# Kernel optimization log

Hardware: AMD Instinct MI355X
Metric: run time of the kernel (lower is better)

The kernel has to match this reference:

```python
import jax, jax.numpy as jnp
import numpy as np


def _mlp(x, W1, b1, W2, b2, W3, b3):
    # flatten -> fc(784,512) -> relu -> fc(512,128) -> relu -> fc(128,C)
    h = x.reshape(x.shape[0], -1)
    h = jax.nn.relu(h @ W1.T + b1)
    h = jax.nn.relu(h @ W2.T + b2)
    return h @ W3.T + b3


def setup_inputs() -> dict:
    key = jax.random.key(0)
    ks = jax.random.split(key, 6)
    B, Bu, C, D = 65536, 4096, 10, 28 * 28
    return {
        "x": jax.random.uniform(ks[0], (B, 28, 28), jnp.float32),
        "y": jax.random.randint(ks[1], (B,), 0, C),
        "x_unlab": jax.random.uniform(ks[2], (Bu, 28, 28), jnp.float32),
        "W1": jax.random.normal(ks[3], (512, D), jnp.float32) * 0.03,
        "b1": jnp.zeros((512,), jnp.float32),
        "W2": jax.random.normal(ks[4], (128, 512), jnp.float32) * 0.05,
        "b2": jnp.zeros((128,), jnp.float32),
        "W3": jax.random.normal(ks[5], (C, 128), jnp.float32) * 0.08,
        "b3": jnp.zeros((C,), jnp.float32),
    }


def reference(x, y, x_unlab, W1, b1, W2, b2, W3, b3):
    n_classes = W3.shape[0]
    # ---- labeled branch: BCEWithLogitsLoss(mean) vs one-hot targets ----
    logits = _mlp(x, W1, b1, W2, b2, W3, b3)  # [B, C]
    t = jax.nn.one_hot(y, n_classes, dtype=logits.dtype)
    bce = jnp.mean(jnp.maximum(logits, 0.0) - logits * t
                   + jnp.log1p(jnp.exp(-jnp.abs(logits))))
    # ---- unlabeled branch: semantic loss ----
    # sem_loss(probs): s[c] = sum_i p_i[c] * prod_{j != i} (1 - p_j[c]);
    # return mean over classes of -log(s). Done in log domain with a single
    # O(Bu) leave-one-out sum instead of the original O(Bu^2) double loop.
    o_u = _mlp(x_unlab, W1, b1, W2, b2, W3, b3)       # [Bu, C]
    logp = jax.nn.log_sigmoid(o_u)                     # log p
    log1mp = jax.nn.log_sigmoid(-o_u)                  # log (1 - p)
    loo = jnp.sum(log1mp, axis=0, keepdims=True) - log1mp  # leave-one-out log-prod
    log_s = jax.scipy.special.logsumexp(logp + loo, axis=0)  # [C]
    sl = jnp.mean(-log_s)
    # compute_loss returns (bce, sl); stacked here as a length-2 vector
    return jnp.stack([bce, sl])
```

## Files before the change

kernel.cpp:

```cpp
#include <hip/hip_runtime.h>
#include <hip/hip_bf16.h>
#include <stdint.h>

typedef unsigned short ushort_t;
typedef __bf16 bf16x8 __attribute__((ext_vector_type(8)));
typedef float f32x4 __attribute__((ext_vector_type(4)));

__device__ __forceinline__ ushort_t f2bf(float f) {
    union { float f; unsigned u; } v; v.f = f;
    unsigned u = v.u;
    unsigned r = u + 0x7fffu + ((u >> 16) & 1u);
    return (ushort_t)(r >> 16);
}
__device__ __forceinline__ float bf2f(ushort_t h) {
    union { unsigned u; float f; } v; v.u = ((unsigned)h) << 16;
    return v.f;
}
__device__ __forceinline__ uint4 pack8(float4 a, float4 b) {
    uint4 r;
    r.x = ((unsigned)f2bf(a.y) << 16) | f2bf(a.x);
    r.y = ((unsigned)f2bf(a.w) << 16) | f2bf(a.z);
    r.z = ((unsigned)f2bf(b.y) << 16) | f2bf(b.x);
    r.w = ((unsigned)f2bf(b.w) << 16) | f2bf(b.z);
    return r;
}

#define GLDS16(gsrc, ldst)                                                    \
    __builtin_amdgcn_global_load_lds(                                         \
        (const __attribute__((address_space(1))) void*)(gsrc),                \
        (__attribute__((address_space(3))) void*)(ldst), 16, 0, 0)

__global__ __launch_bounds__(256) void prep_kernel(
    const float* __restrict__ W1, const float* __restrict__ W2,
    ushort_t* __restrict__ W1p, ushort_t* __restrict__ W2b,
    float* __restrict__ stats)
{
    int idx = blockIdx.x * 256 + threadIdx.x;
    if (idx < 512 * 800) {
        int n = idx / 800, k = idx - n * 800;
        W1p[idx] = (k < 784) ? f2bf(W1[n * 784 + k]) : (ushort_t)0;
    }
    if (idx < 128 * 512) W2b[idx] = f2bf(W2[idx]);
    if (idx == 0) stats[0] = 0.0f;
}

__global__ __launch_bounds__(256) void gemm1f_kernel(
    const float* __restrict__ x, const float* __restrict__ xu,
    const ushort_t* __restrict__ W1p, const float* __restrict__ b1,
    ushort_t* __restrict__ h1)
{
    __shared__ ushort_t As[2][128 * 32];
    __shared__ ushort_t Bs[2][128 * 32];

    const int b = blockIdx.x;
    const int xcd = b & 7, s = b >> 3;
    const int tile_n = s & 3;
    const int tile_m = xcd * 68 + (s >> 2);

    const int tid = threadIdx.x;
    const int w = tid >> 6, lane = tid & 63;
    const int wm = w >> 1, wn = w & 1;
    const int quad = lane >> 4, lc = lane & 15;
    const int row_in = lane >> 2;
    const int koff = (lane & 3) * 8;

    const int arow = tid >> 1;
    const int akoff = (tid & 1) * 16;
    const int grow = tile_m * 128 + arow;
    const float* asrc = (grow < 65536) ? (x + (size_t)grow * 784)
                                       : (xu + (size_t)(grow - 65536) * 784);

    const ushort_t* bsrc0 =
        W1p + (size_t)(tile_n * 128 + (w * 2 + 0) * 16 + row_in) * 800 + koff;
    const ushort_t* bsrc1 =
        W1p + (size_t)(tile_n * 128 + (w * 2 + 1) * 16 + row_in) * 800 + koff;

    f32x4 acc[4][4];
#pragma unroll
    for (int i = 0; i < 4; i++)
#pragma unroll
        for (int j = 0; j < 4; j++)
#pragma unroll
            for (int r = 0; r < 4; r++) acc[i][j][r] = 0.0f;

    float4 pa0, pa1, pa2, pa3;

    GLDS16(bsrc0, &Bs[0][(w * 2 + 0) * 512]);
    GLDS16(bsrc1, &Bs[0][(w * 2 + 1) * 512]);
    {
        const float4* q = (const float4*)(asrc + akoff);
        float4 a0 = q[0], a1 = q[1], a2 = q[2], a3 = q[3];
        *(uint4*)&As[0][arow * 32 + akoff]     = pack8(a0, a1);
        *(uint4*)&As[0][arow * 32 + akoff + 8] = pack8(a2, a3);
    }
    {
        const float4* q = (const float4*)(asrc + 32 + akoff);
        pa0 = q[0]; pa1 = q[1]; pa2 = q[2]; pa3 = q[3];
    }
    __syncthreads();

    for (int t = 0; t < 25; ++t) {
        const int cur = t & 1;
        if (t < 24) {
            ushort_t* Asn = &As[cur ^ 1][0];
            ushort_t* Bsn = &Bs[cur ^ 1][0];
            const int kb = (t + 1) * 32;
            GLDS16(bsrc0 + kb, &Bsn[(w * 2 + 0) * 512]);
            GLDS16(bsrc1 + kb, &Bsn[(w * 2 + 1) * 512]);
            uint4 lo, hi;
            if (kb + akoff <= 768) {
                lo = pack8(pa0, pa1);
                hi = pack8(pa2, pa3);
            } else {
                lo = make_uint4(0, 0, 0, 0);
                hi = make_uint4(0, 0, 0, 0);
            }
            *(uint4*)&Asn[arow * 32 + akoff]     = lo;
            *(uint4*)&Asn[arow * 32 + akoff + 8] = hi;
            const int kn = (t + 2) * 32 + akoff;
            if (t < 23 && kn <= 768) {
                const float4* q = (const float4*)(asrc + kn);
                pa0 = q[0]; pa1 = q[1]; pa2 = q[2]; pa3 = q[3];
            }
        }
        {
            bf16x8 af[4], bfr[4];
#pragma unroll
            for (int i = 0; i < 4; i++)
                af[i] = *(const bf16x8*)&As[cur][(wm * 64 + i * 16 + lc) * 32 + quad * 8];
#pragma unroll
            for (int j = 0; j < 4; j++)
                bfr[j] = *(const bf16x8*)&Bs[cur][(wn * 64 + j * 16 + lc) * 32 + quad * 8];
#pragma unroll
            for (int i = 0; i < 4; i++)
#pragma unroll
                for (int j = 0; j < 4; j++)
                    acc[i][j] = __builtin_amdgcn_mfma_f32_16x16x32_bf16(
                        af[i], bfr[j], acc[i][j], 0, 0, 0);
        }
        if (t < 24) __syncthreads();
    }

    float bias[4];
#pragma unroll
    for (int j = 0; j < 4; j++)
        bias[j] = b1[tile_n * 128 + wn * 64 + j * 16 + lc];
#pragma unroll
    for (int i = 0; i < 4; i++) {
        int gr0 = tile_m * 128 + wm * 64 + i * 16 + quad * 4;
#pragma unroll
        for (int j = 0; j < 4; j++) {
            int gc = tile_n * 128 + wn * 64 + j * 16 + lc;
#pragma unroll
            for (int r = 0; r < 4; r++) {
                float v = acc[i][j][r] + bias[j];
                v = fmaxf(v, 0.0f);
                h1[(size_t)(gr0 + r) * 512 + gc] = f2bf(v);
            }
        }
    }
}

__global__ __launch_bounds__(256) void gemm23_kernel(
    const ushort_t* __restrict__ h1, const ushort_t* __restrict__ W2b,
    const float* __restrict__ b2, const int* __restrict__ y,
    const float* __restrict__ W3, const float* __restrict__ b3,
    float* __restrict__ stats, float* __restrict__ logits_u)
{
    __shared__ ushort_t As[2][64 * 32];
    __shared__ ushort_t Bs[2][128 * 32];
    __shared__ float W3s[1280];
    __shared__ float b3s[10];
    __shared__ float red[4];

    const int tid = threadIdx.x;
    const int w = tid >> 6, lane = tid & 63;
    const int wm = w >> 1, wn = w & 1;
    const int quad = lane >> 4, lc = lane & 15;
    const int row_in = lane >> 2;
    const int koff = (lane & 3) * 8;
    const int tile_m = blockIdx.x;

    for (int i = tid; i < 1280; i += 256) W3s[i] = W3[i];
    if (tid < 10) b3s[tid] = b3[tid];

    const ushort_t* asrc =
        h1 + (size_t)(tile_m * 64 + w * 16 + row_in) * 512 + koff;
    const ushort_t* bsrc0 =
        W2b + (size_t)((w * 2 + 0) * 16 + row_in) * 512 + koff;
    const ushort_t* bsrc1 =
        W2b + (size_t)((w * 2 + 1) * 16 + row_in) * 512 + koff;

    f32x4 acc[2][4];
#pragma unroll
    for (int i = 0; i < 2; i++)
#pragma unroll
        for (int j = 0; j < 4; j++)
#pragma unroll
            for (int r = 0; r < 4; r++) acc[i][j][r] = 0.0f;

    GLDS16(asrc,  &As[0][w * 512]);
    GLDS16(bsrc0, &Bs[0][(w * 2 + 0) * 512]);
    GLDS16(bsrc1, &Bs[0][(w * 2 + 1) * 512]);
    __syncthreads();

    for (int t = 0; t < 16; ++t) {
        const int cur = t & 1;
        if (t < 15) {
            const int kb = (t + 1) * 32;
            GLDS16(asrc + kb,  &As[cur ^ 1][w * 512]);
            GLDS16(bsrc0 + kb, &Bs[cur ^ 1][(w * 2 + 0) * 512]);
            GLDS16(bsrc1 + kb, &Bs[cur ^ 1][(w * 2 + 1) * 512]);
        }
        {
            bf16x8 af[2], bfr[4];
#pragma unroll
            for (int i = 0; i < 2; i++)
                af[i] = *(const bf16x8*)&As[cur][(wm * 32 + i * 16 + lc) * 32 + quad * 8];
#pragma unroll
            for (int j = 0; j < 4; j++)
                bfr[j] = *(const bf16x8*)&Bs[cur][(wn * 64 + j * 16 + lc) * 32 + quad * 8];
#pragma unroll
            for (int i = 0; i < 2; i++)
#pragma unroll
                for (int j = 0; j < 4; j++)
                    acc[i][j] = __builtin_amdgcn_mfma_f32_16x16x32_bf16(
                        af[i], bfr[j], acc[i][j], 0, 0, 0);
        }
        __syncthreads();
    }

    ushort_t* h2s = &Bs[0][0];
    float bias[4];
#pragma unroll
    for (int j = 0; j < 4; j++) bias[j] = b2[wn * 64 + j * 16 + lc];
#pragma unroll
    for (int i = 0; i < 2; i++) {
        int row0 = wm * 32 + i * 16 + quad * 4;
#pragma unroll
        for (int j = 0; j < 4; j++) {
            int col = wn * 64 + j * 16 + lc;
#pragma unroll
            for (int r = 0; r < 4; r++) {
                float v = fmaxf(acc[i][j][r] + bias[j], 0.0f);
                h2s[(row0 + r) * 128 + col] = f2bf(v);
            }
        }
    }
    __syncthreads();

    const size_t row0g = (size_t)tile_m * 64;
    float bce_part = 0.0f;
    for (int o = tid; o < 640; o += 256) {
        int r = o / 10, c = o - r * 10;
        size_t grw = row0g + r;
        float a = b3s[c];
        const ushort_t* hr = &h2s[r * 128];
        const float* wr = &W3s[c * 128];
#pragma unroll 8
        for (int k = 0; k < 128; k++) a += bf2f(hr[k]) * wr[k];
        if (grw < 65536) {
            float t = (y[grw] == c) ? 1.0f : 0.0f;
            bce_part += fmaxf(a, 0.0f) - a * t + log1pf(__expf(-fabsf(a)));
        } else {
            logits_u[(grw - 65536) * 10 + c] = a;
        }
    }
#pragma unroll
    for (int s = 32; s > 0; s >>= 1) bce_part += __shfl_down(bce_part, s, 64);
    if ((tid & 63) == 0) red[tid >> 6] = bce_part;
    __syncthreads();
    if (tid == 0) atomicAdd(stats, red[0] + red[1] + red[2] + red[3]);
}

__global__ __launch_bounds__(640) void finisher_kernel(
    const float* __restrict__ logits_u, const float* __restrict__ stats,
    float* __restrict__ out)
{
    __shared__ float Rs[64][10];
    __shared__ float Rm[64][10];
    __shared__ float Scol[10], Mcol[10];

    const int tid = threadIdx.x;
    const int g = tid / 10, c = tid - g * 10;
    float s = 0.0f, m = -1e30f;
    for (int i = g; i < 4096; i += 64) {
        float o = logits_u[i * 10 + c];
        s += fminf(-o, 0.0f) - log1pf(__expf(-fabsf(o)));
        m = fmaxf(m, o);
    }
    Rs[g][c] = s;
    Rm[g][c] = m;
    __syncthreads();
    if (tid < 10) {
        float ss = 0.0f, mm = -1e30f;
        for (int gg = 0; gg < 64; gg++) {
            ss += Rs[gg][tid];
            mm = fmaxf(mm, Rm[gg][tid]);
        }
        Scol[tid] = ss;
        Mcol[tid] = mm;
    }
    __syncthreads();
    float e = 0.0f;
    float mm = Mcol[c];
    for (int i = g; i < 4096; i += 64)
        e += __expf(logits_u[i * 10 + c] - mm);
    Rs[g][c] = e;
    __syncthreads();
    if (tid == 0) {
        float sl = 0.0f;
        for (int cc = 0; cc < 10; cc++) {
            float ee = 0.0f;
            for (int gg = 0; gg < 64; gg++) ee += Rs[gg][cc];
            sl += -(Scol[cc] + Mcol[cc] + __logf(ee));
        }
        sl *= 0.1f;
        out[0] = stats[0] * (1.0f / (65536.0f * 10.0f));
        out[1] = sl;
    }
}

extern "C" void kernel_launch(void* const* d_in, const int* in_sizes, int n_in,
                              void* d_out, int out_size, void* d_ws,
                              size_t ws_size, hipStream_t stream)
{
    const float* x  = (const float*)d_in[0];
    const int*   y  = (const int*)d_in[1];
    const float* xu = (const float*)d_in[2];
    const float* W1 = (const float*)d_in[3];
    const float* b1 = (const float*)d_in[4];
    const float* W2 = (const float*)d_in[5];
    const float* b2 = (const float*)d_in[6];
    const float* W3 = (const float*)d_in[7];
    const float* b3 = (const float*)d_in[8];
    float* out = (float*)d_out;

    char* ws = (char*)d_ws;
    ushort_t* W1p      = (ushort_t*)(ws + 0);
    ushort_t* W2b      = (ushort_t*)(ws + 819200);
    float*    stats    = (float*)(ws + 950272);
    float*    logits_u = (float*)(ws + 950528);
    ushort_t* h1       = (ushort_t*)(ws + 1114368);

    prep_kernel<<<1600, 256, 0, stream>>>(W1, W2, W1p, W2b, stats);
    gemm1f_kernel<<<2176, 256, 0, stream>>>(x, xu, W1p, b1, h1);
    gemm23_kernel<<<1088, 256, 0, stream>>>(h1, W2b, b2, y, W3, b3, stats,
                                            logits_u);
    finisher_kernel<<<1, 640, 0, stream>>>(logits_u, stats, out);
    (void)in_sizes; (void)n_in; (void)out_size; (void)ws_size;
}
```

Baseline: 502.9 us.

## Use partial vmcnt waits and triple-buffer LDS in GEMM pipelines

Replaces __syncthreads with explicit s_waitcnt vmcnt(N) plus s_barrier in the first GEMM, so the prefetch of the next A tile into registers can stay in flight across the barrier. The second GEMM moves to a three-stage LDS ring that loads two k-steps ahead, also with partial vmcnt waits. The goal is to hide global-load latency behind MFMA work, at the cost of more shared memory (which may lower occupancy) and fragile hand-counted waitcnt values. The last-iteration A prefetch now always issues a load, using a dummy address, to keep the vmcnt count uniform.

New measurement: 525.5 us. 4.5% more time.

```diff
diff --git a/kernel.cpp b/kernel.cpp
--- a/kernel.cpp
+++ b/kernel.cpp
@@ -93,20 +93,21 @@
         *(uint4*)&As[0][arow * 32 + akoff]     = pack8(a0, a1);
         *(uint4*)&As[0][arow * 32 + akoff + 8] = pack8(a2, a3);
     }
+    __builtin_amdgcn_sched_barrier(0);
     {
         const float4* q = (const float4*)(asrc + 32 + akoff);
         pa0 = q[0]; pa1 = q[1]; pa2 = q[2]; pa3 = q[3];
     }
-    __syncthreads();
+    __builtin_amdgcn_sched_barrier(0);
+    asm volatile("s_waitcnt vmcnt(4) lgkmcnt(0)" ::: "memory");
+    __builtin_amdgcn_s_barrier();
 
     for (int t = 0; t < 25; ++t) {
         const int cur = t & 1;
         if (t < 24) {
-            ushort_t* Asn = &As[cur ^ 1][0];
-            ushort_t* Bsn = &Bs[cur ^ 1][0];
             const int kb = (t + 1) * 32;
-            GLDS16(bsrc0 + kb, &Bsn[(w * 2 + 0) * 512]);
-            GLDS16(bsrc1 + kb, &Bsn[(w * 2 + 1) * 512]);
+            GLDS16(bsrc0 + kb, &Bs[cur ^ 1][(w * 2 + 0) * 512]);
+            GLDS16(bsrc1 + kb, &Bs[cur ^ 1][(w * 2 + 1) * 512]);
             uint4 lo, hi;
             if (kb + akoff <= 768) {
                 lo = pack8(pa0, pa1);
@@ -115,13 +116,15 @@
                 lo = make_uint4(0, 0, 0, 0);
                 hi = make_uint4(0, 0, 0, 0);
             }
-            *(uint4*)&Asn[arow * 32 + akoff]     = lo;
-            *(uint4*)&Asn[arow * 32 + akoff + 8] = hi;
-            const int kn = (t + 2) * 32 + akoff;
-            if (t < 23 && kn <= 768) {
-                const float4* q = (const float4*)(asrc + kn);
-                pa0 = q[0]; pa1 = q[1]; pa2 = q[2]; pa3 = q[3];
-            }
+            ushort_t* Asn = &As[cur ^ 1][arow * 32 + akoff];
+            *(uint4*)Asn       = lo;
+            *(uint4*)(Asn + 8) = hi;
+            __builtin_amdgcn_sched_barrier(0);
+            int kn = (t + 2) * 32 + akoff;
+            if (t >= 23 || kn > 768) kn = akoff;
+            const float4* q = (const float4*)(asrc + kn);
+            pa0 = q[0]; pa1 = q[1]; pa2 = q[2]; pa3 = q[3];
+            __builtin_amdgcn_sched_barrier(0);
         }
         {
             bf16x8 af[4], bfr[4];
@@ -138,7 +141,10 @@
                     acc[i][j] = __builtin_amdgcn_mfma_f32_16x16x32_bf16(
                         af[i], bfr[j], acc[i][j], 0, 0, 0);
         }
-        if (t < 24) __syncthreads();
+        if (t < 24) {
+            asm volatile("s_waitcnt vmcnt(4) lgkmcnt(0)" ::: "memory");
+            __builtin_amdgcn_s_barrier();
+        }
     }
 
     float bias[4];
@@ -167,8 +173,8 @@
     const float* __restrict__ W3, const float* __restrict__ b3,
     float* __restrict__ stats, float* __restrict__ logits_u)
 {
-    __shared__ ushort_t As[2][64 * 32];
-    __shared__ ushort_t Bs[2][128 * 32];
+    __shared__ ushort_t As[3][64 * 32];
+    __shared__ ushort_t Bs[3][128 * 32];
     __shared__ float W3s[1280];
     __shared__ float b3s[10];
     __shared__ float red[4];
@@ -183,6 +189,8 @@
 
     for (int i = tid; i < 1280; i += 256) W3s[i] = W3[i];
     if (tid < 10) b3s[tid] = b3[tid];
+    asm volatile("s_waitcnt vmcnt(0)" ::: "memory");
+    __builtin_amdgcn_sched_barrier(0);
 
     const ushort_t* asrc =
         h1 + (size_t)(tile_m * 64 + w * 16 + row_in) * 512 + koff;
@@ -199,27 +207,33 @@
 #pragma unroll
             for (int r = 0; r < 4; r++) acc[i][j][r] = 0.0f;
 
-    GLDS16(asrc,  &As[0][w * 512]);
-    GLDS16(bsrc0, &Bs[0][(w * 2 + 0) * 512]);
-    GLDS16(bsrc1, &Bs[0][(w * 2 + 1) * 512]);
-    __syncthreads();
+    GLDS16(asrc,       &As[0][w * 512]);
+    GLDS16(bsrc0,      &Bs[0][(w * 2 + 0) * 512]);
+    GLDS16(bsrc1,      &Bs[0][(w * 2 + 1) * 512]);
+    GLDS16(asrc + 32,  &As[1][w * 512]);
+    GLDS16(bsrc0 + 32, &Bs[1][(w * 2 + 0) * 512]);
+    GLDS16(bsrc1 + 32, &Bs[1][(w * 2 + 1) * 512]);
+    asm volatile("s_waitcnt vmcnt(3) lgkmcnt(0)" ::: "memory");
+    __builtin_amdgcn_s_barrier();
 
     for (int t = 0; t < 16; ++t) {
-        const int cur = t & 1;
-        if (t < 15) {
-            const int kb = (t + 1) * 32;
-            GLDS16(asrc + kb,  &As[cur ^ 1][w * 512]);
-            GLDS16(bsrc0 + kb, &Bs[cur ^ 1][(w * 2 + 0) * 512]);
-            GLDS16(bsrc1 + kb, &Bs[cur ^ 1][(w * 2 + 1) * 512]);
-        }
+        const int bcur = t % 3;
+        if (t < 14) {
+            const int kb = (t + 2) * 32;
+            const int bnx = (t + 2) % 3;
+            GLDS16(asrc + kb,  &As[bnx][w * 512]);
+            GLDS16(bsrc0 + kb, &Bs[bnx][(w * 2 + 0) * 512]);
+            GLDS16(bsrc1 + kb, &Bs[bnx][(w * 2 + 1) * 512]);
+        }
+        __builtin_amdgcn_sched_barrier(0);
         {
             bf16x8 af[2], bfr[4];
 #pragma unroll
             for (int i = 0; i < 2; i++)
-                af[i] = *(const bf16x8*)&As[cur][(wm * 32 + i * 16 + lc) * 32 + quad * 8];
+                af[i] = *(const bf16x8*)&As[bcur][(wm * 32 + i * 16 + lc) * 32 + quad * 8];
 #pragma unroll
             for (int j = 0; j < 4; j++)
-                bfr[j] = *(const bf16x8*)&Bs[cur][(wn * 64 + j * 16 + lc) * 32 + quad * 8];
+                bfr[j] = *(const bf16x8*)&Bs[bcur][(wn * 64 + j * 16 + lc) * 32 + quad * 8];
 #pragma unroll
             for (int i = 0; i < 2; i++)
 #pragma unroll
@@ -227,7 +241,16 @@
                     acc[i][j] = __builtin_amdgcn_mfma_f32_16x16x32_bf16(
                         af[i], bfr[j], acc[i][j], 0, 0, 0);
         }
-        __syncthreads();
+        if (t < 14) {
+            asm volatile("s_waitcnt vmcnt(3) lgkmcnt(0)" ::: "memory");
+            __builtin_amdgcn_s_barrier();
+        } else if (t == 14) {
+            asm volatile("s_waitcnt vmcnt(0) lgkmcnt(0)" ::: "memory");
+            __builtin_amdgcn_s_barrier();
+        } else {
+            asm volatile("s_waitcnt lgkmcnt(0)" ::: "memory");
+            __builtin_amdgcn_s_barrier();
+        }
     }
 
     ushort_t* h2s = &Bs[0][0];
```
